# Kernel optimization log

Measured on AMD Instinct MI355X. Metric: run time of the kernel, lower is better.

The kernel has to match this reference:

```python
import jax, jax.numpy as jnp
import numpy as np

ALPHA = 0.1
K = 5


def setup_inputs() -> dict:
    key = jax.random.key(0)
    ks = jax.random.split(key, 6)
    N, E = 50000, 800000
    IN, HID, OUT = 512, 256, 64
    x = jax.random.normal(ks[0], (N, IN), dtype=jnp.float32)
    edge_index = jax.random.randint(ks[1], (2, E), 0, N, dtype=jnp.int64)
    # Linear params (torch Linear: y = x @ W.T + b), kaiming-ish scale
    W1 = jax.random.normal(ks[2], (HID, IN), dtype=jnp.float32) / np.sqrt(IN)
    b1 = jnp.zeros((HID,), dtype=jnp.float32)
    W2 = jax.random.normal(ks[3], (OUT, HID), dtype=jnp.float32) / np.sqrt(HID)
    b2 = jnp.zeros((OUT,), dtype=jnp.float32)
    return {"x": x, "W1": W1, "b1": b1, "W2": W2, "b2": b2,
            "edge_index": edge_index}


def reference(x, W1, b1, W2, b2, edge_index):
    N = x.shape[0]
    # --- MLP encoder (eval mode: dropout is identity) ---
    h = jax.nn.relu(x @ W1.T + b1)          # [N, HID]
    h = h @ W2.T + b2                       # [N, OUT]

    # --- gcn_norm with self-loops (PyG APPNP default) ---
    src, dst = edge_index[0], edge_index[1]
    loop = jnp.arange(N, dtype=src.dtype)
    src_f = jnp.concatenate([src, loop])    # [E+N]
    dst_f = jnp.concatenate([dst, loop])
    ew = jnp.ones(src_f.shape[0], dtype=h.dtype)
    deg = jax.ops.segment_sum(ew, dst_f, num_segments=N)
    dinv = jnp.where(deg > 0, jax.lax.rsqrt(deg), 0.0)
    norm = dinv[src_f] * dinv[dst_f]        # [E+N]

    # --- K iterations of personalized-PageRank propagation ---
    def body(xk, _):
        msg = norm[:, None] * xk[src_f]                      # gather [E+N, OUT]
        agg = jax.ops.segment_sum(msg, dst_f, num_segments=N)
        return (1.0 - ALPHA) * agg + ALPHA * h, None

    xK, _ = jax.lax.scan(body, h, None, length=K)
    return jax.nn.log_softmax(xK, axis=1)
```

## Files before the change

kernel.cpp:

```cpp
#include <hip/hip_runtime.h>
#include <hip/hip_bf16.h>

#define IN_DIM  512
#define HID_DIM 256
#define OUT_DIM 64

typedef __attribute__((ext_vector_type(8))) short bf16x8;
typedef __attribute__((ext_vector_type(4))) float f32x4;

static __device__ __forceinline__ ushort f2b(float f) {
    __hip_bfloat16 b = __float2bfloat16(f);
    return *reinterpret_cast<ushort*>(&b);
}
static __device__ __forceinline__ float b2f_lo(uint u) {
    union { uint u; float f; } t; t.u = u << 16; return t.f;
}
static __device__ __forceinline__ float b2f_hi(uint u) {
    union { uint u; float f; } t; t.u = u & 0xFFFF0000u; return t.f;
}
static __device__ __forceinline__ uint packbf(float x, float y) {
    return (uint)f2b(x) | ((uint)f2b(y) << 16);
}

#define GLOAD16(g, l) __builtin_amdgcn_global_load_lds(                      \
    (const __attribute__((address_space(1))) void*)(g),                      \
    (__attribute__((address_space(3))) void*)(l), 16, 0, 0)


__global__ __launch_bounds__(256) void f2b_kernel(const float* __restrict__ in,
                                                  ushort* __restrict__ out, int n8) {
    for (int i = blockIdx.x * 256 + threadIdx.x; i < n8; i += gridDim.x * 256) {
        float4 a = *reinterpret_cast<const float4*>(&in[(size_t)i * 8]);
        float4 b = *reinterpret_cast<const float4*>(&in[(size_t)i * 8 + 4]);
        ushort4 lo = make_ushort4(f2b(a.x), f2b(a.y), f2b(a.z), f2b(a.w));
        ushort4 hi = make_ushort4(f2b(b.x), f2b(b.y), f2b(b.z), f2b(b.w));
        *reinterpret_cast<ushort4*>(&out[(size_t)i * 8])     = lo;
        *reinterpret_cast<ushort4*>(&out[(size_t)i * 8 + 4]) = hi;
    }
}


__global__ void hist_kernel(const int* __restrict__ ei, int* __restrict__ deg, int E) {
    int e = blockIdx.x * 256 + threadIdx.x;
    if (e < E) atomicAdd(&deg[ei[E + e]], 1);
}


__global__ __launch_bounds__(256) void scanA_kernel(const int* __restrict__ deg,
                                                    int* __restrict__ offs,
                                                    int* __restrict__ bsum, int N) {
    __shared__ int sh[256];
    int tid = threadIdx.x;
    int i = blockIdx.x * 256 + tid;
    int v = (i < N) ? deg[i] : 0;
    sh[tid] = v;
    __syncthreads();
#pragma unroll
    for (int off = 1; off < 256; off <<= 1) {
        int t = (tid >= off) ? sh[tid - off] : 0;
        __syncthreads();
        sh[tid] += t;
        __syncthreads();
    }
    if (i < N) offs[i] = sh[tid] - v;
    if (tid == 255) bsum[blockIdx.x] = sh[255];
}

__global__ __launch_bounds__(256) void scanB_kernel(int* __restrict__ bsum, int nb) {
    __shared__ int sh[256];
    int tid = threadIdx.x;
    int v = (tid < nb) ? bsum[tid] : 0;
    sh[tid] = v;
    __syncthreads();
#pragma unroll
    for (int off = 1; off < 256; off <<= 1) {
        int t = (tid >= off) ? sh[tid - off] : 0;
        __syncthreads();
        sh[tid] += t;
        __syncthreads();
    }
    if (tid < nb) bsum[tid] = sh[tid] - v;
}

__global__ __launch_bounds__(256) void scanC_kernel(const int* __restrict__ deg,
                                                    const int* __restrict__ bsum,
                                                    int* __restrict__ offs,
                                                    float* __restrict__ dinv,
                                                    int N, int E) {
    int i = blockIdx.x * 256 + threadIdx.x;
    if (i < N) {
        offs[i] += bsum[i >> 8];
        dinv[i] = rsqrtf((float)(deg[i] + 1));
    }
    if (i == 0) offs[N] = E;
}

__global__ void fill_kernel(const int* __restrict__ ei, const int* __restrict__ offs,
                            int* __restrict__ cursor, const float* __restrict__ dinv,
                            int2* __restrict__ edat, int E) {
    int e = blockIdx.x * 256 + threadIdx.x;
    if (e < E) {
        int s = ei[e];
        int d = ei[E + e];
        int pos = offs[d] + atomicAdd(&cursor[d], 1);
        edat[pos] = make_int2(s, __float_as_int(dinv[d] * dinv[s]));
    }
}


__global__ __launch_bounds__(256) void gemm1_mfma(const ushort* __restrict__ A,
                                                  const ushort* __restrict__ B,
                                                  const float* __restrict__ bias,
                                                  ushort* __restrict__ C, int M) {
    constexpr int K = IN_DIM;
    constexpr int NK = K / 64;
    __shared__ ushort As[128 * 64];
    __shared__ ushort Bs[128 * 64];

    const int tid  = threadIdx.x;
    const int lane = tid & 63;
    const int wid  = tid >> 6;
    const int wm = wid >> 1, wn = wid & 1;
    const int m0 = blockIdx.y * 128;
    const int n0 = blockIdx.x * 128;
    const int l15 = lane & 15;
    const int lq  = lane >> 4;

    const int srow = lane >> 3;
    const int sslot = (lane & 7) ^ srow;

    f32x4 acc[4][4];
#pragma unroll
    for (int i = 0; i < 4; ++i)
#pragma unroll
        for (int j = 0; j < 4; ++j) acc[i][j] = (f32x4)0.0f;

    for (int ks = 0; ks < NK; ++ks) {
        const int k0 = ks * 64;
#pragma unroll
        for (int q = 0; q < 4; ++q) {
            const int rbase = (wid * 4 + q) * 8;
            const int row = rbase + srow;
            int am = m0 + row; if (am >= M) am = M - 1;
            const ushort* ga = A + (size_t)am * K + k0 + sslot * 8;
            const ushort* gb = B + (size_t)(n0 + row) * K + k0 + sslot * 8;
            GLOAD16(ga, &As[rbase * 64]);
            GLOAD16(gb, &Bs[rbase * 64]);
        }
        __syncthreads();
#pragma unroll
        for (int kk = 0; kk < 2; ++kk) {
            bf16x8 af[4], bf[4];
#pragma unroll
            for (int f = 0; f < 4; ++f) {
                const int ar = wm * 64 + f * 16 + l15;
                const int br = wn * 64 + f * 16 + l15;
                const int slot = kk * 4 + lq;
                af[f] = *reinterpret_cast<const bf16x8*>(&As[ar * 64 + (slot ^ (ar & 7)) * 8]);
                bf[f] = *reinterpret_cast<const bf16x8*>(&Bs[br * 64 + (slot ^ (br & 7)) * 8]);
            }
#pragma unroll
            for (int i = 0; i < 4; ++i)
#pragma unroll
                for (int j = 0; j < 4; ++j)
                    acc[i][j] = __builtin_amdgcn_mfma_f32_16x16x32_bf16(af[i], bf[j], acc[i][j], 0, 0, 0);
        }
        __syncthreads();
    }

    const int lr = lq * 4;
#pragma unroll
    for (int nf = 0; nf < 4; ++nf) {
        int col = n0 + wn * 64 + nf * 16 + l15;
        float bv = bias[col];
#pragma unroll
        for (int mf = 0; mf < 4; ++mf) {
#pragma unroll
            for (int j = 0; j < 4; ++j) {
                int row = m0 + wm * 64 + mf * 16 + lr + j;
                if (row < M) {
                    float v = fmaxf(acc[mf][nf][j] + bv, 0.f);
                    C[(size_t)row * HID_DIM + col] = f2b(v);
                }
            }
        }
    }
}


#define LDT 40

__global__ __launch_bounds__(256) void gemm2_bf16(const ushort* __restrict__ A,
                                                  const float* __restrict__ B,
                                                  const float* __restrict__ bias,
                                                  float* __restrict__ C,
                                                  int M) {
    constexpr int K = HID_DIM;
    constexpr int NK = K / 32;
    __shared__ ushort As[128 * LDT];
    __shared__ ushort Bs[64 * LDT];

    const int tid = threadIdx.x;
    const int lane = tid & 63;
    const int wid = tid >> 6;
    const int wm = wid >> 1, wn = wid & 1;
    const int m0 = blockIdx.x * 128;
    const int l15 = lane & 15;
    const int koff = (lane >> 4) * 8;

    f32x4 acc[4][2];
#pragma unroll
    for (int i = 0; i < 4; ++i)
#pragma unroll
        for (int j = 0; j < 2; ++j) acc[i][j] = (f32x4)0.0f;

    uint4 rawA[2];
    float4 rbv[2];
#pragma unroll
    for (int i = 0; i < 2; ++i) {
        int slot = tid + i * 256;
        int rowA = slot >> 2, c8 = (slot & 3) << 3;
        int m = m0 + rowA;
        rawA[i] = (m < M) ? *reinterpret_cast<const uint4*>(&A[(size_t)m * K + c8])
                          : make_uint4(0u, 0u, 0u, 0u);
        int rowB = slot >> 3, c4 = (slot & 7) << 2;
        rbv[i] = *reinterpret_cast<const float4*>(&B[(size_t)rowB * K + c4]);
    }
#pragma unroll
    for (int i = 0; i < 2; ++i) {
        int slot = tid + i * 256;
        int rowA = slot >> 2, c8 = (slot & 3) << 3;
        *reinterpret_cast<uint4*>(&As[rowA * LDT + c8]) = rawA[i];
        int rowB = slot >> 3, c4 = (slot & 7) << 2;
        ushort4 ub = make_ushort4(f2b(rbv[i].x), f2b(rbv[i].y), f2b(rbv[i].z), f2b(rbv[i].w));
        *reinterpret_cast<ushort4*>(&Bs[rowB * LDT + c4]) = ub;
    }
    __syncthreads();

    for (int ks = 0; ks < NK; ++ks) {
        if (ks + 1 < NK) {
            int k0 = (ks + 1) * 32;
#pragma unroll
            for (int i = 0; i < 2; ++i) {
                int slot = tid + i * 256;
                int rowA = slot >> 2, c8 = (slot & 3) << 3;
                int m = m0 + rowA;
                rawA[i] = (m < M) ? *reinterpret_cast<const uint4*>(&A[(size_t)m * K + k0 + c8])
                                  : make_uint4(0u, 0u, 0u, 0u);
                int rowB = slot >> 3, c4 = (slot & 7) << 2;
                rbv[i] = *reinterpret_cast<const float4*>(&B[(size_t)rowB * K + k0 + c4]);
            }
        }
        bf16x8 af[4], bf[2];
#pragma unroll
        for (int f = 0; f < 4; ++f)
            af[f] = *reinterpret_cast<const bf16x8*>(&As[(wm * 64 + f * 16 + l15) * LDT + koff]);
#pragma unroll
        for (int f = 0; f < 2; ++f)
            bf[f] = *reinterpret_cast<const bf16x8*>(&Bs[(wn * 32 + f * 16 + l15) * LDT + koff]);
#pragma unroll
        for (int i = 0; i < 4; ++i)
#pragma unroll
            for (int j = 0; j < 2; ++j)
                acc[i][j] = __builtin_amdgcn_mfma_f32_16x16x32_bf16(af[i], bf[j], acc[i][j], 0, 0, 0);
        __syncthreads();
        if (ks + 1 < NK) {
#pragma unroll
            for (int i = 0; i < 2; ++i) {
                int slot = tid + i * 256;
                int rowA = slot >> 2, c8 = (slot & 3) << 3;
                *reinterpret_cast<uint4*>(&As[rowA * LDT + c8]) = rawA[i];
                int rowB = slot >> 3, c4 = (slot & 7) << 2;
                ushort4 ub = make_ushort4(f2b(rbv[i].x), f2b(rbv[i].y), f2b(rbv[i].z), f2b(rbv[i].w));
                *reinterpret_cast<ushort4*>(&Bs[rowB * LDT + c4]) = ub;
            }
            __syncthreads();
        }
    }

    const int lr = (lane >> 4) * 4;
#pragma unroll
    for (int nf = 0; nf < 2; ++nf) {
        int col = wn * 32 + nf * 16 + l15;
        float bv = bias[col];
#pragma unroll
        for (int mf = 0; mf < 4; ++mf) {
#pragma unroll
            for (int j = 0; j < 4; ++j) {
                int row = m0 + wm * 64 + mf * 16 + lr + j;
                if (row < M)
                    C[(size_t)row * OUT_DIM + col] = acc[mf][nf][j] + bv;
            }
        }
    }
}


__global__ __launch_bounds__(256) void propb_kernel(const uint* __restrict__ xin,
                                                    const float* __restrict__ h,
                                                    const float* __restrict__ dinv,
                                                    const int* __restrict__ offs,
                                                    const int2* __restrict__ edat,
                                                    uint* __restrict__ xout, int N) {
    int node = blockIdx.x * 4 + (threadIdx.x >> 6);
    int lane = threadIdx.x & 63;
    if (node >= N) return;
    const int l32 = lane & 31;
    const int hi  = lane >> 5;
    int e0 = offs[node], e1 = offs[node + 1];

    float ax[4] = {0.f, 0.f, 0.f, 0.f};
    float ay[4] = {0.f, 0.f, 0.f, 0.f};
    int e = e0;
    for (; e + 8 <= e1; e += 8) {
#pragma unroll
        for (int i = 0; i < 4; ++i) {
            int2 ed = edat[e + 2 * i + hi];
            uint g = xin[(size_t)ed.x * 32 + l32];
            float w = __int_as_float(ed.y);
            ax[i] = fmaf(w, b2f_lo(g), ax[i]);
            ay[i] = fmaf(w, b2f_hi(g), ay[i]);
        }
    }
    for (; e + 2 <= e1; e += 2) {
        int2 ed = edat[e + hi];
        uint g = xin[(size_t)ed.x * 32 + l32];
        float w = __int_as_float(ed.y);
        ax[0] = fmaf(w, b2f_lo(g), ax[0]);
        ay[0] = fmaf(w, b2f_hi(g), ay[0]);
    }
    if (e < e1 && hi == 0) {
        int2 ed = edat[e];
        uint g = xin[(size_t)ed.x * 32 + l32];
        float w = __int_as_float(ed.y);
        ax[1] = fmaf(w, b2f_lo(g), ax[1]);
        ay[1] = fmaf(w, b2f_hi(g), ay[1]);
    }
    float sx = (ax[0] + ax[1]) + (ax[2] + ax[3]);
    float sy = (ay[0] + ay[1]) + (ay[2] + ay[3]);
    sx += __shfl_xor(sx, 32);
    sy += __shfl_xor(sy, 32);
    float di = dinv[node];
    uint gs = xin[(size_t)node * 32 + l32];
    sx = fmaf(di * di, b2f_lo(gs), sx);
    sy = fmaf(di * di, b2f_hi(gs), sy);
    float2 hv = *reinterpret_cast<const float2*>(&h[(size_t)node * 64 + l32 * 2]);
    float r0 = 0.9f * sx + 0.1f * hv.x;
    float r1 = 0.9f * sy + 0.1f * hv.y;
    if (hi == 0) xout[(size_t)node * 32 + l32] = packbf(r0, r1);
}


__global__ __launch_bounds__(256) void propb_lsm_kernel(const uint* __restrict__ xin,
                                                        const float* __restrict__ h,
                                                        const float* __restrict__ dinv,
                                                        const int* __restrict__ offs,
                                                        const int2* __restrict__ edat,
                                                        float* __restrict__ out, int N) {
    int node = blockIdx.x * 4 + (threadIdx.x >> 6);
    int lane = threadIdx.x & 63;
    if (node >= N) return;
    const int l32 = lane & 31;
    const int hi  = lane >> 5;
    int e0 = offs[node], e1 = offs[node + 1];

    float ax[4] = {0.f, 0.f, 0.f, 0.f};
    float ay[4] = {0.f, 0.f, 0.f, 0.f};
    int e = e0;
    for (; e + 8 <= e1; e += 8) {
#pragma unroll
        for (int i = 0; i < 4; ++i) {
            int2 ed = edat[e + 2 * i + hi];
            uint g = xin[(size_t)ed.x * 32 + l32];
            float w = __int_as_float(ed.y);
            ax[i] = fmaf(w, b2f_lo(g), ax[i]);
            ay[i] = fmaf(w, b2f_hi(g), ay[i]);
        }
    }
    for (; e + 2 <= e1; e += 2) {
        int2 ed = edat[e + hi];
        uint g = xin[(size_t)ed.x * 32 + l32];
        float w = __int_as_float(ed.y);
        ax[0] = fmaf(w, b2f_lo(g), ax[0]);
        ay[0] = fmaf(w, b2f_hi(g), ay[0]);
    }
    if (e < e1 && hi == 0) {
        int2 ed = edat[e];
        uint g = xin[(size_t)ed.x * 32 + l32];
        float w = __int_as_float(ed.y);
        ax[1] = fmaf(w, b2f_lo(g), ax[1]);
        ay[1] = fmaf(w, b2f_hi(g), ay[1]);
    }
    float sx = (ax[0] + ax[1]) + (ax[2] + ax[3]);
    float sy = (ay[0] + ay[1]) + (ay[2] + ay[3]);
    sx += __shfl_xor(sx, 32);
    sy += __shfl_xor(sy, 32);
    float di = dinv[node];
    uint gs = xin[(size_t)node * 32 + l32];
    sx = fmaf(di * di, b2f_lo(gs), sx);
    sy = fmaf(di * di, b2f_hi(gs), sy);
    float2 hv = *reinterpret_cast<const float2*>(&h[(size_t)node * 64 + l32 * 2]);
    float r0 = 0.9f * sx + 0.1f * hv.x;
    float r1 = 0.9f * sy + 0.1f * hv.y;

    float m = fmaxf(r0, r1);
    for (int o = 16; o > 0; o >>= 1) m = fmaxf(m, __shfl_xor(m, o));
    float sum = expf(r0 - m) + expf(r1 - m);
    for (int o = 16; o > 0; o >>= 1) sum += __shfl_xor(sum, o);
    float ls = logf(sum);
    if (hi == 0) {
        float2 o2 = make_float2(r0 - m - ls, r1 - m - ls);
        *reinterpret_cast<float2*>(&out[(size_t)node * 64 + l32 * 2]) = o2;
    }
}


static inline size_t align256(size_t x) { return (x + 255) & ~(size_t)255; }

extern "C" void kernel_launch(void* const* d_in, const int* in_sizes, int n_in,
                              void* d_out, int out_size, void* d_ws, size_t ws_size,
                              hipStream_t stream) {
    const float* x  = (const float*)d_in[0];
    const float* W1 = (const float*)d_in[1];
    const float* b1 = (const float*)d_in[2];
    const float* W2 = (const float*)d_in[3];
    const float* b2 = (const float*)d_in[4];
    const int*   ei = (const int*)d_in[5];

    const int N = in_sizes[0] / IN_DIM;
    const int E = in_sizes[5] / 2;
    const int nb = (N + 255) / 256;

    char* base = (char*)d_ws;
    size_t off = 0;
    ushort* xb  = (ushort*)(base + off); off += align256((size_t)N * IN_DIM * 2);
    ushort* w1b = (ushort*)(base + off); off += align256((size_t)HID_DIM * IN_DIM * 2);
    ushort* h1  = (ushort*)(base + off); off += align256((size_t)N * HID_DIM * 2);
    float* h    = (float*)(base + off);  off += align256((size_t)N * OUT_DIM * 4);
    float* dinv = (float*)(base + off);  off += align256((size_t)N * 4);
    int*   deg  = (int*)(base + off);    off += align256((size_t)N * 4);
    int*   offs = (int*)(base + off);    off += align256((size_t)(N + 1) * 4);
    int*   cur  = (int*)(base + off);    off += align256((size_t)N * 4);
    int*   bsum = (int*)(base + off);    off += align256((size_t)nb * 4);
    int2*  edat = (int2*)(base + off);   off += align256((size_t)E * 8);

    uint* hb  = (uint*)xb;
    uint* xsa = hb  + (size_t)N * 32;
    uint* xsb = xsa + (size_t)N * 32;

    hipMemsetAsync(deg, 0, (size_t)N * 4, stream);
    hipMemsetAsync(cur, 0, (size_t)N * 4, stream);
    hist_kernel<<<(E + 255) / 256, 256, 0, stream>>>(ei, deg, E);
    scanA_kernel<<<nb, 256, 0, stream>>>(deg, offs, bsum, N);
    scanB_kernel<<<1, 256, 0, stream>>>(bsum, nb);
    scanC_kernel<<<nb, 256, 0, stream>>>(deg, bsum, offs, dinv, N, E);
    fill_kernel<<<(E + 255) / 256, 256, 0, stream>>>(ei, offs, cur, dinv, edat, E);

    f2b_kernel<<<2048, 256, 0, stream>>>(x, xb, N * IN_DIM / 8);
    f2b_kernel<<<64, 256, 0, stream>>>(W1, w1b, HID_DIM * IN_DIM / 8);

    {
        dim3 g(HID_DIM / 128, (N + 127) / 128);
        gemm1_mfma<<<g, 256, 0, stream>>>(xb, w1b, b1, h1, N);
    }
    {
        dim3 g((N + 127) / 128);
        gemm2_bf16<<<g, 256, 0, stream>>>(h1, W2, b2, h, N);
    }

    f2b_kernel<<<2048, 256, 0, stream>>>(h, (ushort*)hb, N * OUT_DIM / 8);

    int blocks = (N + 3) / 4;
    propb_kernel<<<blocks, 256, 0, stream>>>(hb,  h, dinv, offs, edat, xsa, N);
    propb_kernel<<<blocks, 256, 0, stream>>>(xsa, h, dinv, offs, edat, xsb, N);
    propb_kernel<<<blocks, 256, 0, stream>>>(xsb, h, dinv, offs, edat, xsa, N);
    propb_kernel<<<blocks, 256, 0, stream>>>(xsa, h, dinv, offs, edat, xsb, N);
    propb_lsm_kernel<<<blocks, 256, 0, stream>>>(xsb, h, dinv, offs, edat,
                                                 (float*)d_out, N);
}
```

Measured before the change: 329.4 us.

## Fuse x conversion into GEMM1, pack edges to 32-bit, use bf16 h, half-wave propagation

GEMM1 now loads fp32 x straight into LDS and converts it to bf16 in registers, which removes the separate x-to-bf16 pass and its extra traffic. GEMM2 writes h directly as bf16, so the later f2b pass is gone and propagation reads bf16 h. Edge records are packed into 32 bits (16-bit source index plus a bf16 weight), halving edge traffic, and each node is now handled by 32 lanes with 8 independent gathers in flight instead of a split 64-lane scheme. The risks are that the 16-bit index only works while N is below 65536, and that the bf16 weights and h lose precision.

After: 281.9 us. -14.4%, faster.

```diff
diff --git a/kernel.cpp b/kernel.cpp
--- a/kernel.cpp
+++ b/kernel.cpp
@@ -45,7 +45,6 @@
     if (e < E) atomicAdd(&deg[ei[E + e]], 1);
 }
 
-
 __global__ __launch_bounds__(256) void scanA_kernel(const int* __restrict__ deg,
                                                     int* __restrict__ offs,
                                                     int* __restrict__ bsum, int N) {
@@ -97,24 +96,24 @@
 
 __global__ void fill_kernel(const int* __restrict__ ei, const int* __restrict__ offs,
                             int* __restrict__ cursor, const float* __restrict__ dinv,
-                            int2* __restrict__ edat, int E) {
+                            uint* __restrict__ edat, int E) {
     int e = blockIdx.x * 256 + threadIdx.x;
     if (e < E) {
         int s = ei[e];
         int d = ei[E + e];
         int pos = offs[d] + atomicAdd(&cursor[d], 1);
-        edat[pos] = make_int2(s, __float_as_int(dinv[d] * dinv[s]));
-    }
-}
-
-
-__global__ __launch_bounds__(256) void gemm1_mfma(const ushort* __restrict__ A,
+        edat[pos] = (uint)s | ((uint)f2b(dinv[d] * dinv[s]) << 16);
+    }
+}
+
+
+__global__ __launch_bounds__(256) void gemm1_f32a(const float* __restrict__ A,
                                                   const ushort* __restrict__ B,
                                                   const float* __restrict__ bias,
                                                   ushort* __restrict__ C, int M) {
     constexpr int K = IN_DIM;
     constexpr int NK = K / 64;
-    __shared__ ushort As[128 * 64];
+    __shared__ float  Asf[128 * 64];
     __shared__ ushort Bs[128 * 64];
 
     const int tid  = threadIdx.x;
@@ -126,7 +125,10 @@
     const int l15 = lane & 15;
     const int lq  = lane >> 4;
 
-    const int srow = lane >> 3;
+    const int a_r   = lane >> 4;
+    const int a_s16 = lane & 15;
+    const int a_pair = a_s16 >> 1, a_sub = a_s16 & 1;
+    const int srow  = lane >> 3;
     const int sslot = (lane & 7) ^ srow;
 
     f32x4 acc[4][4];
@@ -141,23 +143,37 @@
         for (int q = 0; q < 4; ++q) {
             const int rbase = (wid * 4 + q) * 8;
             const int row = rbase + srow;
+            const ushort* gb = B + (size_t)(n0 + row) * K + k0 + sslot * 8;
+            GLOAD16(gb, &Bs[rbase * 64]);
+        }
+#pragma unroll
+        for (int q = 0; q < 8; ++q) {
+            const int rbase = (wid * 8 + q) * 4;
+            const int row = rbase + a_r;
             int am = m0 + row; if (am >= M) am = M - 1;
-            const ushort* ga = A + (size_t)am * K + k0 + sslot * 8;
-            const ushort* gb = B + (size_t)(n0 + row) * K + k0 + sslot * 8;
-            GLOAD16(ga, &As[rbase * 64]);
-            GLOAD16(gb, &Bs[rbase * 64]);
+            const int col = k0 + ((a_pair ^ (row & 7)) << 3) + (a_sub << 2);
+            const float* ga = A + (size_t)am * K + col;
+            GLOAD16(ga, &Asf[rbase * 64]);
         }
         __syncthreads();
 #pragma unroll
         for (int kk = 0; kk < 2; ++kk) {
+            const int p = kk * 4 + lq;
             bf16x8 af[4], bf[4];
 #pragma unroll
             for (int f = 0; f < 4; ++f) {
                 const int ar = wm * 64 + f * 16 + l15;
+                const int fi = ar * 64 + ((p ^ (ar & 7)) << 3);
+                f32x4 v0 = *reinterpret_cast<const f32x4*>(&Asf[fi]);
+                f32x4 v1 = *reinterpret_cast<const f32x4*>(&Asf[fi + 4]);
+                bf16x8 a;
+                a[0] = (short)f2b(v0[0]); a[1] = (short)f2b(v0[1]);
+                a[2] = (short)f2b(v0[2]); a[3] = (short)f2b(v0[3]);
+                a[4] = (short)f2b(v1[0]); a[5] = (short)f2b(v1[1]);
+                a[6] = (short)f2b(v1[2]); a[7] = (short)f2b(v1[3]);
+                af[f] = a;
                 const int br = wn * 64 + f * 16 + l15;
-                const int slot = kk * 4 + lq;
-                af[f] = *reinterpret_cast<const bf16x8*>(&As[ar * 64 + (slot ^ (ar & 7)) * 8]);
-                bf[f] = *reinterpret_cast<const bf16x8*>(&Bs[br * 64 + (slot ^ (br & 7)) * 8]);
+                bf[f] = *reinterpret_cast<const bf16x8*>(&Bs[br * 64 + ((p ^ (br & 7)) << 3)]);
             }
 #pragma unroll
             for (int i = 0; i < 4; ++i)
@@ -193,7 +209,7 @@
 __global__ __launch_bounds__(256) void gemm2_bf16(const ushort* __restrict__ A,
                                                   const float* __restrict__ B,
                                                   const float* __restrict__ bias,
-                                                  float* __restrict__ C,
+                                                  ushort* __restrict__ Cb,
                                                   int M) {
     constexpr int K = HID_DIM;
     constexpr int NK = K / 32;
@@ -289,7 +305,7 @@
             for (int j = 0; j < 4; ++j) {
                 int row = m0 + wm * 64 + mf * 16 + lr + j;
                 if (row < M)
-                    C[(size_t)row * OUT_DIM + col] = acc[mf][nf][j] + bv;
+                    Cb[(size_t)row * OUT_DIM + col] = f2b(acc[mf][nf][j] + bv);
             }
         }
     }
@@ -297,121 +313,115 @@
 
 
 __global__ __launch_bounds__(256) void propb_kernel(const uint* __restrict__ xin,
-                                                    const float* __restrict__ h,
+                                                    const uint* __restrict__ hb,
                                                     const float* __restrict__ dinv,
                                                     const int* __restrict__ offs,
-                                                    const int2* __restrict__ edat,
+                                                    const uint* __restrict__ edat,
                                                     uint* __restrict__ xout, int N) {
-    int node = blockIdx.x * 4 + (threadIdx.x >> 6);
-    int lane = threadIdx.x & 63;
+    int node = blockIdx.x * 8 + (threadIdx.x >> 5);
+    int l32 = threadIdx.x & 31;
     if (node >= N) return;
-    const int l32 = lane & 31;
-    const int hi  = lane >> 5;
     int e0 = offs[node], e1 = offs[node + 1];
 
     float ax[4] = {0.f, 0.f, 0.f, 0.f};
     float ay[4] = {0.f, 0.f, 0.f, 0.f};
     int e = e0;
     for (; e + 8 <= e1; e += 8) {
-#pragma unroll
-        for (int i = 0; i < 4; ++i) {
-            int2 ed = edat[e + 2 * i + hi];
-            uint g = xin[(size_t)ed.x * 32 + l32];
-            float w = __int_as_float(ed.y);
-            ax[i] = fmaf(w, b2f_lo(g), ax[i]);
-            ay[i] = fmaf(w, b2f_hi(g), ay[i]);
-        }
-    }
-    for (; e + 2 <= e1; e += 2) {
-        int2 ed = edat[e + hi];
-        uint g = xin[(size_t)ed.x * 32 + l32];
-        float w = __int_as_float(ed.y);
-        ax[0] = fmaf(w, b2f_lo(g), ax[0]);
-        ay[0] = fmaf(w, b2f_hi(g), ay[0]);
-    }
-    if (e < e1 && hi == 0) {
-        int2 ed = edat[e];
-        uint g = xin[(size_t)ed.x * 32 + l32];
-        float w = __int_as_float(ed.y);
-        ax[1] = fmaf(w, b2f_lo(g), ax[1]);
-        ay[1] = fmaf(w, b2f_hi(g), ay[1]);
+        uint p0 = edat[e+0], p1 = edat[e+1], p2 = edat[e+2], p3 = edat[e+3];
+        uint p4 = edat[e+4], p5 = edat[e+5], p6 = edat[e+6], p7 = edat[e+7];
+        uint g0 = xin[(size_t)(p0 & 0xFFFFu) * 32 + l32];
+        uint g1 = xin[(size_t)(p1 & 0xFFFFu) * 32 + l32];
+        uint g2 = xin[(size_t)(p2 & 0xFFFFu) * 32 + l32];
+        uint g3 = xin[(size_t)(p3 & 0xFFFFu) * 32 + l32];
+        uint g4 = xin[(size_t)(p4 & 0xFFFFu) * 32 + l32];
+        uint g5 = xin[(size_t)(p5 & 0xFFFFu) * 32 + l32];
+        uint g6 = xin[(size_t)(p6 & 0xFFFFu) * 32 + l32];
+        uint g7 = xin[(size_t)(p7 & 0xFFFFu) * 32 + l32];
+        ax[0] = fmaf(b2f_hi(p0), b2f_lo(g0), ax[0]); ay[0] = fmaf(b2f_hi(p0), b2f_hi(g0), ay[0]);
+        ax[1] = fmaf(b2f_hi(p1), b2f_lo(g1), ax[1]); ay[1] = fmaf(b2f_hi(p1), b2f_hi(g1), ay[1]);
+        ax[2] = fmaf(b2f_hi(p2), b2f_lo(g2), ax[2]); ay[2] = fmaf(b2f_hi(p2), b2f_hi(g2), ay[2]);
+        ax[3] = fmaf(b2f_hi(p3), b2f_lo(g3), ax[3]); ay[3] = fmaf(b2f_hi(p3), b2f_hi(g3), ay[3]);
+        ax[0] = fmaf(b2f_hi(p4), b2f_lo(g4), ax[0]); ay[0] = fmaf(b2f_hi(p4), b2f_hi(g4), ay[0]);
+        ax[1] = fmaf(b2f_hi(p5), b2f_lo(g5), ax[1]); ay[1] = fmaf(b2f_hi(p5), b2f_hi(g5), ay[1]);
+        ax[2] = fmaf(b2f_hi(p6), b2f_lo(g6), ax[2]); ay[2] = fmaf(b2f_hi(p6), b2f_hi(g6), ay[2]);
+        ax[3] = fmaf(b2f_hi(p7), b2f_lo(g7), ax[3]); ay[3] = fmaf(b2f_hi(p7), b2f_hi(g7), ay[3]);
+    }
+    for (; e < e1; ++e) {
+        uint p = edat[e];
+        uint g = xin[(size_t)(p & 0xFFFFu) * 32 + l32];
+        ax[0] = fmaf(b2f_hi(p), b2f_lo(g), ax[0]);
+        ay[0] = fmaf(b2f_hi(p), b2f_hi(g), ay[0]);
     }
     float sx = (ax[0] + ax[1]) + (ax[2] + ax[3]);
     float sy = (ay[0] + ay[1]) + (ay[2] + ay[3]);
-    sx += __shfl_xor(sx, 32);
-    sy += __shfl_xor(sy, 32);
     float di = dinv[node];
     uint gs = xin[(size_t)node * 32 + l32];
     sx = fmaf(di * di, b2f_lo(gs), sx);
     sy = fmaf(di * di, b2f_hi(gs), sy);
-    float2 hv = *reinterpret_cast<const float2*>(&h[(size_t)node * 64 + l32 * 2]);
-    float r0 = 0.9f * sx + 0.1f * hv.x;
-    float r1 = 0.9f * sy + 0.1f * hv.y;
-    if (hi == 0) xout[(size_t)node * 32 + l32] = packbf(r0, r1);
+    uint ah = hb[(size_t)node * 32 + l32];
+    float r0 = 0.9f * sx + 0.1f * b2f_lo(ah);
+    float r1 = 0.9f * sy + 0.1f * b2f_hi(ah);
+    xout[(size_t)node * 32 + l32] = packbf(r0, r1);
 }
 
 
 __global__ __launch_bounds__(256) void propb_lsm_kernel(const uint* __restrict__ xin,
-                                                        const float* __restrict__ h,
+                                                        const uint* __restrict__ hb,
                                                         const float* __restrict__ dinv,
                                                         const int* __restrict__ offs,
-                                                        const int2* __restrict__ edat,
+                                                        const uint* __restrict__ edat,
                                                         float* __restrict__ out, int N) {
-    int node = blockIdx.x * 4 + (threadIdx.x >> 6);
-    int lane = threadIdx.x & 63;
+    int node = blockIdx.x * 8 + (threadIdx.x >> 5);
+    int l32 = threadIdx.x & 31;
     if (node >= N) return;
-    const int l32 = lane & 31;
-    const int hi  = lane >> 5;
     int e0 = offs[node], e1 = offs[node + 1];
 
     float ax[4] = {0.f, 0.f, 0.f, 0.f};
     float ay[4] = {0.f, 0.f, 0.f, 0.f};
     int e = e0;
     for (; e + 8 <= e1; e += 8) {
-#pragma unroll
-        for (int i = 0; i < 4; ++i) {
-            int2 ed = edat[e + 2 * i + hi];
-            uint g = xin[(size_t)ed.x * 32 + l32];
-            float w = __int_as_float(ed.y);
-            ax[i] = fmaf(w, b2f_lo(g), ax[i]);
-            ay[i] = fmaf(w, b2f_hi(g), ay[i]);
-        }
-    }
-    for (; e + 2 <= e1; e += 2) {
-        int2 ed = edat[e + hi];
-        uint g = xin[(size_t)ed.x * 32 + l32];
-        float w = __int_as_float(ed.y);
-        ax[0] = fmaf(w, b2f_lo(g), ax[0]);
-        ay[0] = fmaf(w, b2f_hi(g), ay[0]);
-    }
-    if (e < e1 && hi == 0) {
-        int2 ed = edat[e];
-        uint g = xin[(size_t)ed.x * 32 + l32];
-        float w = __int_as_float(ed.y);
-        ax[1] = fmaf(w, b2f_lo(g), ax[1]);
-        ay[1] = fmaf(w, b2f_hi(g), ay[1]);
+        uint p0 = edat[e+0], p1 = edat[e+1], p2 = edat[e+2], p3 = edat[e+3];
+        uint p4 = edat[e+4], p5 = edat[e+5], p6 = edat[e+6], p7 = edat[e+7];
+        uint g0 = xin[(size_t)(p0 & 0xFFFFu) * 32 + l32];
+        uint g1 = xin[(size_t)(p1 & 0xFFFFu) * 32 + l32];
+        uint g2 = xin[(size_t)(p2 & 0xFFFFu) * 32 + l32];
+        uint g3 = xin[(size_t)(p3 & 0xFFFFu) * 32 + l32];
+        uint g4 = xin[(size_t)(p4 & 0xFFFFu) * 32 + l32];
+        uint g5 = xin[(size_t)(p5 & 0xFFFFu) * 32 + l32];
+        uint g6 = xin[(size_t)(p6 & 0xFFFFu) * 32 + l32];
+        uint g7 = xin[(size_t)(p7 & 0xFFFFu) * 32 + l32];
+        ax[0] = fmaf(b2f_hi(p0), b2f_lo(g0), ax[0]); ay[0] = fmaf(b2f_hi(p0), b2f_hi(g0), ay[0]);
+        ax[1] = fmaf(b2f_hi(p1), b2f_lo(g1), ax[1]); ay[1] = fmaf(b2f_hi(p1), b2f_hi(g1), ay[1]);
+        ax[2] = fmaf(b2f_hi(p2), b2f_lo(g2), ax[2]); ay[2] = fmaf(b2f_hi(p2), b2f_hi(g2), ay[2]);
+        ax[3] = fmaf(b2f_hi(p3), b2f_lo(g3), ax[3]); ay[3] = fmaf(b2f_hi(p3), b2f_hi(g3), ay[3]);
+        ax[0] = fmaf(b2f_hi(p4), b2f_lo(g4), ax[0]); ay[0] = fmaf(b2f_hi(p4), b2f_hi(g4), ay[0]);
+        ax[1] = fmaf(b2f_hi(p5), b2f_lo(g5), ax[1]); ay[1] = fmaf(b2f_hi(p5), b2f_hi(g5), ay[1]);
+        ax[2] = fmaf(b2f_hi(p6), b2f_lo(g6), ax[2]); ay[2] = fmaf(b2f_hi(p6), b2f_hi(g6), ay[2]);
+        ax[3] = fmaf(b2f_hi(p7), b2f_lo(g7), ax[3]); ay[3] = fmaf(b2f_hi(p7), b2f_hi(g7), ay[3]);
+    }
+    for (; e < e1; ++e) {
+        uint p = edat[e];
+        uint g = xin[(size_t)(p & 0xFFFFu) * 32 + l32];
+        ax[0] = fmaf(b2f_hi(p), b2f_lo(g), ax[0]);
+        ay[0] = fmaf(b2f_hi(p), b2f_hi(g), ay[0]);
     }
     float sx = (ax[0] + ax[1]) + (ax[2] + ax[3]);
     float sy = (ay[0] + ay[1]) + (ay[2] + ay[3]);
-    sx += __shfl_xor(sx, 32);
-    sy += __shfl_xor(sy, 32);
     float di = dinv[node];
     uint gs = xin[(size_t)node * 32 + l32];
     sx = fmaf(di * di, b2f_lo(gs), sx);
     sy = fmaf(di * di, b2f_hi(gs), sy);
-    float2 hv = *reinterpret_cast<const float2*>(&h[(size_t)node * 64 + l32 * 2]);
-    float r0 = 0.9f * sx + 0.1f * hv.x;
-    float r1 = 0.9f * sy + 0.1f * hv.y;
+    uint ah = hb[(size_t)node * 32 + l32];
+    float r0 = 0.9f * sx + 0.1f * b2f_lo(ah);
+    float r1 = 0.9f * sy + 0.1f * b2f_hi(ah);
 
     float m = fmaxf(r0, r1);
     for (int o = 16; o > 0; o >>= 1) m = fmaxf(m, __shfl_xor(m, o));
     float sum = expf(r0 - m) + expf(r1 - m);
     for (int o = 16; o > 0; o >>= 1) sum += __shfl_xor(sum, o);
     float ls = logf(sum);
-    if (hi == 0) {
-        float2 o2 = make_float2(r0 - m - ls, r1 - m - ls);
-        *reinterpret_cast<float2*>(&out[(size_t)node * 64 + l32 * 2]) = o2;
-    }
+    float2 o2 = make_float2(r0 - m - ls, r1 - m - ls);
+    *reinterpret_cast<float2*>(&out[(size_t)node * 64 + l32 * 2]) = o2;
 }
 
 
@@ -433,20 +443,17 @@
 
     char* base = (char*)d_ws;
     size_t off = 0;
-    ushort* xb  = (ushort*)(base + off); off += align256((size_t)N * IN_DIM * 2);
+    uint*  hb  = (uint*)(base + off);    off += align256((size_t)N * 32 * 4);
+    uint*  xsa = (uint*)(base + off);    off += align256((size_t)N * 32 * 4);
+    uint*  xsb = (uint*)(base + off);    off += align256((size_t)N * 32 * 4);
     ushort* w1b = (ushort*)(base + off); off += align256((size_t)HID_DIM * IN_DIM * 2);
     ushort* h1  = (ushort*)(base + off); off += align256((size_t)N * HID_DIM * 2);
-    float* h    = (float*)(base + off);  off += align256((size_t)N * OUT_DIM * 4);
     float* dinv = (float*)(base + off);  off += align256((size_t)N * 4);
     int*   deg  = (int*)(base + off);    off += align256((size_t)N * 4);
     int*   offs = (int*)(base + off);    off += align256((size_t)(N + 1) * 4);
     int*   cur  = (int*)(base + off);    off += align256((size_t)N * 4);
     int*   bsum = (int*)(base + off);    off += align256((size_t)nb * 4);
-    int2*  edat = (int2*)(base + off);   off += align256((size_t)E * 8);
-
-    uint* hb  = (uint*)xb;
-    uint* xsa = hb  + (size_t)N * 32;
-    uint* xsb = xsa + (size_t)N * 32;
+    uint*  edat = (uint*)(base + off);   off += align256((size_t)E * 4);
 
     hipMemsetAsync(deg, 0, (size_t)N * 4, stream);
     hipMemsetAsync(cur, 0, (size_t)N * 4, stream);
@@ -456,25 +463,22 @@
     scanC_kernel<<<nb, 256, 0, stream>>>(deg, bsum, offs, dinv, N, E);
     fill_kernel<<<(E + 255) / 256, 256, 0, stream>>>(ei, offs, cur, dinv, edat, E);
 
-    f2b_kernel<<<2048, 256, 0, stream>>>(x, xb, N * IN_DIM / 8);
     f2b_kernel<<<64, 256, 0, stream>>>(W1, w1b, HID_DIM * IN_DIM / 8);
 
     {
         dim3 g(HID_DIM / 128, (N + 127) / 128);
-        gemm1_mfma<<<g, 256, 0, stream>>>(xb, w1b, b1, h1, N);
+        gemm1_f32a<<<g, 256, 0, stream>>>(x, w1b, b1, h1, N);
     }
     {
         dim3 g((N + 127) / 128);
-        gemm2_bf16<<<g, 256, 0, stream>>>(h1, W2, b2, h, N);
-    }
-
-    f2b_kernel<<<2048, 256, 0, stream>>>(h, (ushort*)hb, N * OUT_DIM / 8);
-
-    int blocks = (N + 3) / 4;
-    propb_kernel<<<blocks, 256, 0, stream>>>(hb,  h, dinv, offs, edat, xsa, N);
-    propb_kernel<<<blocks, 256, 0, stream>>>(xsa, h, dinv, offs, edat, xsb, N);
-    propb_kernel<<<blocks, 256, 0, stream>>>(xsb, h, dinv, offs, edat, xsa, N);
-    propb_kernel<<<blocks, 256, 0, stream>>>(xsa, h, dinv, offs, edat, xsb, N);
-    propb_lsm_kernel<<<blocks, 256, 0, stream>>>(xsb, h, dinv, offs, edat,
+        gemm2_bf16<<<g, 256, 0, stream>>>(h1, W2, b2, (ushort*)hb, N);
+    }
+
+    int blocks = (N + 7) / 8;
+    propb_kernel<<<blocks, 256, 0, stream>>>(hb,  hb, dinv, offs, edat, xsa, N);
+    propb_kernel<<<blocks, 256, 0, stream>>>(xsa, hb, dinv, offs, edat, xsb, N);
+    propb_kernel<<<blocks, 256, 0, stream>>>(xsb, hb, dinv, offs, edat, xsa, N);
+    propb_kernel<<<blocks, 256, 0, stream>>>(xsa, hb, dinv, offs, edat, xsb, N);
+    propb_lsm_kernel<<<blocks, 256, 0, stream>>>(xsb, hb, dinv, offs, edat,
                                                  (float*)d_out, N);
 }
```
